# Optimization experiments

Measured on AMD Instinct MI355X. Metric: run time of the kernel, lower is better.

## Reference

```python
import jax, jax.numpy as jnp
import numpy as np

D_MODEL, D_INNER, D_STATE, DT_RANK, D_CONV = 1024, 2048, 16, 64, 4
BATCH, SEQLEN = 2, 2048


def setup_inputs() -> dict:
    key = jax.random.key(0)
    ks = jax.random.split(key, 8)
    g = lambda k, shape, scale: jax.random.normal(k, shape, jnp.float32) * scale
    hidden_states = jax.random.normal(ks[0], (BATCH, SEQLEN, D_MODEL), jnp.float32)
    W_in = g(ks[1], (2 * D_INNER, D_MODEL), D_MODEL ** -0.5)
    conv_w = g(ks[2], (D_INNER, D_CONV), D_CONV ** -0.5)
    conv_b = jnp.zeros((D_INNER,), jnp.float32)
    W_x = g(ks[3], (DT_RANK + 2 * D_STATE, D_INNER), D_INNER ** -0.5)
    dt_init_std = DT_RANK ** -0.5  # dt_scale = 1.0
    W_dt = jax.random.uniform(ks[4], (D_INNER, DT_RANK), jnp.float32, -dt_init_std, dt_init_std)
    # faithful dt bias init: softplus^{-1}(dt) with dt ~ LogUniform(dt_min, dt_max)
    dt = jnp.exp(jax.random.uniform(ks[5], (D_INNER,), jnp.float32)
                 * (np.log(0.1) - np.log(0.001)) + np.log(0.001))
    dt = jnp.clip(dt, 1e-4)
    b_dt = dt + jnp.log(-jnp.expm1(-dt))
    A_log = jnp.log(jnp.broadcast_to(jnp.arange(1, D_STATE + 1, dtype=jnp.float32), (D_INNER, D_STATE)))
    D_param = jnp.ones((D_INNER,), jnp.float32)
    W_out = g(ks[6], (D_MODEL, D_INNER), D_INNER ** -0.5)
    return dict(hidden_states=hidden_states, W_in=W_in, conv_w=conv_w, conv_b=conv_b,
                W_x=W_x, W_dt=W_dt, b_dt=b_dt, A_log=A_log, D_param=D_param, W_out=W_out)


def reference(hidden_states, W_in, conv_w, conv_b, W_x, W_dt, b_dt, A_log, D_param, W_out):
    B_, L, _ = hidden_states.shape
    # in_proj (no bias) then split into x / gate z
    xz = jnp.einsum('bld,ed->ble', hidden_states, W_in)  # (B, L, 2*d_inner)
    x, z = jnp.split(xz, 2, axis=-1)
    # depthwise causal conv1d (padding = d_conv - 1, truncated to L)
    xp = jnp.pad(x, ((0, 0), (D_CONV - 1, 0), (0, 0)))
    xc = conv_b + sum(conv_w[:, k] * xp[:, k:k + L, :] for k in range(D_CONV))
    x = jax.nn.silu(xc)  # (B, L, d_inner)
    # input-dependent SSM params
    A = -jnp.exp(A_log)  # (d_inner, d_state)
    proj = jnp.einsum('bld,ed->ble', x, W_x)
    dt_lo, Bm, Cm = jnp.split(proj, [DT_RANK, DT_RANK + D_STATE], axis=-1)
    dt = jax.nn.softplus(jnp.einsum('blr,dr->bld', dt_lo, W_dt) + b_dt)  # (B, L, d_inner)
    # sequential selective scan: h = exp(dt*A)*h + dt*B*x ; y = C.h + D*x
    def step(h, inp):
        x_t, dt_t, B_t, C_t = inp  # (B,d), (B,d), (B,n), (B,n)
        dA = jnp.exp(dt_t[..., None] * A)                       # (B, d, n)
        h = dA * h + (dt_t * x_t)[..., None] * B_t[:, None, :]  # (B, d, n)
        y_t = jnp.einsum('bdn,bn->bd', h, C_t)
        return h, y_t

    h0 = jnp.zeros((B_, D_INNER, D_STATE), x.dtype)
    xs = (x.swapaxes(0, 1), dt.swapaxes(0, 1), Bm.swapaxes(0, 1), Cm.swapaxes(0, 1))
    _, ys = jax.lax.scan(step, h0, xs)
    y = ys.swapaxes(0, 1) + D_param * x
    y = y * jax.nn.silu(z)
    return jnp.einsum('bld,md->blm', y, W_out)
```

## Files before the change

### kernel.cpp

```cpp
#include <hip/hip_runtime.h>

typedef _Float16 f16;
typedef f16   f16x2 __attribute__((ext_vector_type(2)));
typedef f16   f16x4 __attribute__((ext_vector_type(4)));
typedef f16   f16x8 __attribute__((ext_vector_type(8)));
typedef float f32x2 __attribute__((ext_vector_type(2)));
typedef float f32x4 __attribute__((ext_vector_type(4)));

#define LOG2E 1.44269504088896f

__device__ __forceinline__ float fast_exp(float x) {
    return __builtin_amdgcn_exp2f(x * LOG2E);
}
__device__ __forceinline__ float silu_f(float x) {
    return x / (1.f + __builtin_amdgcn_exp2f(-LOG2E * x));
}
__device__ __forceinline__ float softplus_f(float x) {
    if (x > 16.f) return x;
    float e = __builtin_amdgcn_exp2f(x * LOG2E);
    return __builtin_amdgcn_logf(1.f + e) * 0.69314718056f;
}

#define DPP_ADD(x, ctrl) \
    ((x) + __int_as_float(__builtin_amdgcn_update_dpp(0, __float_as_int(x), (ctrl), 0xF, 0xF, true)))

__device__ __forceinline__ void gload_lds16(const void* g, void* l) {
    __builtin_amdgcn_global_load_lds((__attribute__((address_space(1))) void*)(g),
                                     (__attribute__((address_space(3))) void*)(l), 16, 0, 0);
}

__global__ __launch_bounds__(256) void cvt_all(const float* __restrict__ hidden, const float* __restrict__ W_in,
                                               const float* __restrict__ W_out, const float* __restrict__ W_dt,
                                               const float* __restrict__ W_x,
                                               f16* __restrict__ h16, f16* __restrict__ Win16,
                                               f16* __restrict__ Wout16, f16* __restrict__ Wdt16,
                                               f16* __restrict__ Wx16) {
    int i = blockIdx.x * 256 + threadIdx.x;
    const float* src;
    f16* dst;
    int idx;
    if (i < 1048576) { src = hidden; dst = h16; idx = i; }
    else if (i < 2097152) { src = W_in; dst = Win16; idx = i - 1048576; }
    else if (i < 2621440) { src = W_out; dst = Wout16; idx = i - 2097152; }
    else if (i < 2654208) { src = W_dt; dst = Wdt16; idx = i - 2621440; }
    else {
        int q = i - 2654208;
        int r = q >> 9;
        f32x4 v = {0.f, 0.f, 0.f, 0.f};
        if (r < 96) v = ((const f32x4*)W_x)[q];
        f16x4 o = {(f16)v[0], (f16)v[1], (f16)v[2], (f16)v[3]};
        ((f16x4*)Wx16)[q] = o;
        return;
    }
    f32x4 v = ((const f32x4*)src)[idx];
    f16x4 o = {(f16)v[0], (f16)v[1], (f16)v[2], (f16)v[3]};
    ((f16x4*)dst)[idx] = o;
}

__global__ void reduce_proj(const f16* __restrict__ Pws, float* __restrict__ proj,
                            f16* __restrict__ dtlo) {
    int i = blockIdx.x * 256 + threadIdx.x;
    int m = i >> 5, c0 = (i & 31) * 4;
    f32x4 s = {0.f, 0.f, 0.f, 0.f};
#pragma unroll
    for (int z = 0; z < 8; z++) {
        f16x4 p = *(const f16x4*)(Pws + (size_t)z * 4096 * 128 + (size_t)m * 128 + c0);
        s += (f32x4){(float)p[0], (float)p[1], (float)p[2], (float)p[3]};
    }
    *(f32x4*)(proj + (size_t)m * 128 + c0) = s;
    if (c0 < 64) {
        f16x4 o = {(f16)s[0], (f16)s[1], (f16)s[2], (f16)s[3]};
        *(f16x4*)(dtlo + (size_t)m * 64 + c0) = o;
    }
}

__global__ __launch_bounds__(1024) void gemm256(const f16* __restrict__ A, const f16* __restrict__ B,
                                                f16* __restrict__ C, int N, int K) {
    __shared__ f16 As[4][256 * 32];
    __shared__ f16 Bs[4][256 * 32];
    const int tid = threadIdx.x;
    const int w = tid >> 6, l = tid & 63;
    const int wr = w >> 2, wc = w & 3;
    const int lrow = l & 15, lkb = l >> 4;
    const int gpos = ((lkb ^ ((lrow >> 1) & 3)) * 8);
    const int bid = blockIdx.y * 16 + blockIdx.x;
    const int wg = (bid & 7) * 32 + (bid >> 3);
    const int mt = wg >> 4, nt = wg & 15;
    const int NT = K >> 5;

    f32x4 acc[4][4];
#pragma unroll
    for (int i = 0; i < 4; i++)
#pragma unroll
        for (int j = 0; j < 4; j++) acc[i][j] = (f32x4){0.f, 0.f, 0.f, 0.f};

    const int srow = w * 16 + (l >> 2);
    const int sgran = (l & 3) ^ ((l >> 3) & 3);
    const f16* Ag = A + (size_t)(mt * 256 + srow) * K + sgran * 8;
    const f16* Bg = B + (size_t)(nt * 256 + srow) * K + sgran * 8;

#define SCALL(s, kt, q)                                        \
    do {                                                       \
        if ((q) == 0) gload_lds16(Ag + (kt), &As[s][w * 512]); \
        if ((q) == 1) gload_lds16(Bg + (kt), &Bs[s][w * 512]); \
    } while (0)

    SCALL(0, 0, 0); SCALL(0, 0, 1);
    SCALL(1, 32, 0); SCALL(1, 32, 1);
    SCALL(2, 64, 0); SCALL(2, 64, 1);

    for (int t = 0; t < NT; ++t) {
        const f16* as = As[t & 3];
        const f16* bs = Bs[t & 3];
        const int pslot = (t + 3) & 3;
        const int pkt = ((t + 3 < NT) ? (t + 3) : (NT - 1)) * 32;

        asm volatile("s_waitcnt vmcnt(4)" ::: "memory");
        __builtin_amdgcn_sched_barrier(0);
        __builtin_amdgcn_s_barrier();
        __builtin_amdgcn_sched_barrier(0);

        f16x8 af[4], bf[4];
#pragma unroll
        for (int i = 0; i < 4; i++)
            af[i] = *(const f16x8*)&as[(wr * 64 + i * 16 + lrow) * 32 + gpos];
#pragma unroll
        for (int j = 0; j < 4; j++)
            bf[j] = *(const f16x8*)&bs[(wc * 64 + j * 16 + lrow) * 32 + gpos];
        SCALL(pslot, pkt, 0);
        SCALL(pslot, pkt, 1);
        __builtin_amdgcn_s_barrier();
        __builtin_amdgcn_sched_barrier(0);
        __builtin_amdgcn_s_setprio(1);
#pragma unroll
        for (int i = 0; i < 4; i++)
#pragma unroll
            for (int j = 0; j < 4; j++)
                acc[i][j] = __builtin_amdgcn_mfma_f32_16x16x32_f16(af[i], bf[j], acc[i][j], 0, 0, 0);
        __builtin_amdgcn_s_setprio(0);
    }
#undef SCALL

    const int orow = mt * 256 + wr * 64 + (l >> 4) * 4;
    const int ocol = nt * 256 + wc * 64 + lrow;
#pragma unroll
    for (int i = 0; i < 4; i++)
#pragma unroll
        for (int j = 0; j < 4; j++)
#pragma unroll
            for (int q = 0; q < 4; q++)
                C[(size_t)(orow + i * 16 + q) * N + ocol + j * 16] = (f16)acc[i][j][q];
}

__global__ __launch_bounds__(512) void gemm_o32(const f16* __restrict__ A, const f16* __restrict__ B,
                                                float* __restrict__ C, int N, int K) {
    __shared__ f16 As[4][128 * 32];
    __shared__ f16 Bs[4][128 * 32];
    const int tid = threadIdx.x;
    const int w = tid >> 6, l = tid & 63;
    const int wr = w >> 2, wc = w & 3;
    const int lrow = l & 15, lkb = l >> 4;
    const int gpos = ((lkb ^ ((lrow >> 1) & 3)) * 8);
    const int bid = blockIdx.y * 8 + blockIdx.x;
    const int wg = (bid & 7) * 32 + (bid >> 3);
    const int nt = wg & 7, mt = wg >> 3;
    const int NT = K >> 5;

    f32x4 acc[4][2];
#pragma unroll
    for (int i = 0; i < 4; i++)
#pragma unroll
        for (int j = 0; j < 2; j++) acc[i][j] = (f32x4){0.f, 0.f, 0.f, 0.f};

    const int srow = w * 16 + (l >> 2);
    const int sgran = (l & 3) ^ ((l >> 3) & 3);
    const f16* Ag = A + (size_t)(mt * 128 + srow) * K + sgran * 8;
    const f16* Bg = B + (size_t)(nt * 128 + srow) * K + sgran * 8;

#define QCALL(s, kt, q)                                        \
    do {                                                       \
        if ((q) == 0) gload_lds16(Ag + (kt), &As[s][w * 512]); \
        if ((q) == 1) gload_lds16(Bg + (kt), &Bs[s][w * 512]); \
    } while (0)

    QCALL(0, 0, 0); QCALL(0, 0, 1);
    QCALL(1, 32, 0); QCALL(1, 32, 1);
    QCALL(2, 64, 0); QCALL(2, 64, 1);

    for (int t = 0; t < NT; ++t) {
        const f16* as = As[t & 3];
        const f16* bs = Bs[t & 3];
        const int pslot = (t + 3) & 3;
        const int pkt = ((t + 3 < NT) ? (t + 3) : (NT - 1)) * 32;

        asm volatile("s_waitcnt vmcnt(4)" ::: "memory");
        __builtin_amdgcn_sched_barrier(0);
        __builtin_amdgcn_s_barrier();
        __builtin_amdgcn_sched_barrier(0);

        f16x8 af[4], bf[2];
#pragma unroll
        for (int i = 0; i < 4; i++)
            af[i] = *(const f16x8*)&as[(wr * 64 + i * 16 + lrow) * 32 + gpos];
#pragma unroll
        for (int j = 0; j < 2; j++)
            bf[j] = *(const f16x8*)&bs[(wc * 32 + j * 16 + lrow) * 32 + gpos];
        QCALL(pslot, pkt, 0);
        QCALL(pslot, pkt, 1);
        __builtin_amdgcn_s_barrier();
        __builtin_amdgcn_sched_barrier(0);
        __builtin_amdgcn_s_setprio(1);
#pragma unroll
        for (int i = 0; i < 4; i++)
#pragma unroll
            for (int j = 0; j < 2; j++)
                acc[i][j] = __builtin_amdgcn_mfma_f32_16x16x32_f16(af[i], bf[j], acc[i][j], 0, 0, 0);
        __builtin_amdgcn_s_setprio(0);
    }
#undef QCALL

    const int orow = mt * 128 + wr * 64 + (l >> 4) * 4;
    const int ocol = nt * 128 + wc * 32 + lrow;
#pragma unroll
    for (int i = 0; i < 4; i++)
#pragma unroll
        for (int j = 0; j < 2; j++)
#pragma unroll
            for (int q = 0; q < 4; q++)
                C[(size_t)(orow + i * 16 + q) * N + ocol + j * 16] = acc[i][j][q];
}

template <int EPI, typename OutT>
__global__ __launch_bounds__(256) void gemm_gl(const f16* __restrict__ A, const f16* __restrict__ B,
                                               OutT* __restrict__ C, const float* __restrict__ bias,
                                               int M, int N, int K, int kstep) {
    __shared__ f16 As[2][128 * 64];
    __shared__ f16 Bs[2][128 * 64];
    const int tid = threadIdx.x;
    const int w = tid >> 6, l = tid & 63;
    const int wm = (w >> 1) * 64, wn = (w & 1) * 64;
    const int lrow = l & 15, lkb = l >> 4;
    const int swzr = lrow & 7;
    const int gx = gridDim.x;
    const int nwg = gx * gridDim.y;
    const int bid = blockIdx.y * gx + blockIdx.x;
    const int wg = (bid & 7) * (nwg >> 3) + (bid >> 3);
    const int nt = wg % gx, mt = wg / gx;
    const int kbeg = blockIdx.z * kstep;
    const int NT = kstep >> 6;
    OutT* Cz = C + (size_t)blockIdx.z * M * N;

    f32x4 acc[4][4];
#pragma unroll
    for (int i = 0; i < 4; i++)
#pragma unroll
        for (int j = 0; j < 4; j++) acc[i][j] = (f32x4){0.f, 0.f, 0.f, 0.f};

    const int srow = w * 32 + (l >> 3);
    const int sgran = (l & 7) ^ (l >> 3);
    const f16* Ag = A + (size_t)(mt * 128 + srow) * K + sgran * 8 + kbeg;
    const f16* Bg = B + (size_t)(nt * 128 + srow) * K + sgran * 8 + kbeg;

#define STAGE128(s, kt)                                                         \
    do {                                                                        \
        _Pragma("unroll")                                                       \
        for (int i = 0; i < 4; ++i) {                                           \
            gload_lds16(Ag + (size_t)(i * 8) * K + (kt), &As[s][(w * 32 + i * 8) * 64]); \
            gload_lds16(Bg + (size_t)(i * 8) * K + (kt), &Bs[s][(w * 32 + i * 8) * 64]); \
        }                                                                       \
    } while (0)

    STAGE128(0, 0);
    __syncthreads();

    int cur = 0;
    for (int t = 0; t < NT; ++t) {
        if (t + 1 < NT) STAGE128(cur ^ 1, (t + 1) * 64);
#pragma unroll
        for (int kk = 0; kk < 64; kk += 32) {
            f16x8 af[4], bf[4];
            const int g = (kk >> 3) + lkb;
#pragma unroll
            for (int i = 0; i < 4; i++) {
                af[i] = *(const f16x8*)&As[cur][(wm + i * 16 + lrow) * 64 + ((g ^ swzr) * 8)];
                bf[i] = *(const f16x8*)&Bs[cur][(wn + i * 16 + lrow) * 64 + ((g ^ swzr) * 8)];
            }
#pragma unroll
            for (int i = 0; i < 4; i++)
#pragma unroll
                for (int j = 0; j < 4; j++)
                    acc[i][j] = __builtin_amdgcn_mfma_f32_16x16x32_f16(af[i], bf[j], acc[i][j], 0, 0, 0);
        }
        __syncthreads();
        cur ^= 1;
    }
#undef STAGE128

    const int orow = mt * 128 + wm + (l >> 4) * 4;
    const int ocol = nt * 128 + wn + lrow;
#pragma unroll
    for (int fm = 0; fm < 4; fm++)
#pragma unroll
        for (int fn = 0; fn < 4; fn++) {
            int c = ocol + fn * 16;
            float bv = (EPI == 1) ? bias[c] : 0.f;
#pragma unroll
            for (int i = 0; i < 4; i++) {
                float v = acc[fm][fn][i];
                if (EPI == 1) v = softplus_f(v + bv);
                Cz[(size_t)(orow + fm * 16 + i) * N + c] = (OutT)v;
            }
        }
}

__global__ __launch_bounds__(256) void conv_silu_k(const f16* __restrict__ xz, const float* __restrict__ cw,
                                                   const float* __restrict__ cb, f16* __restrict__ xc) {
    const int d0 = threadIdx.x * 8;
    const int g = blockIdx.x;
    const int b = g >> 9;
    const int l0 = (g & 511) * 4;
    const size_t mrow = (size_t)b * 2048 + l0;
    f32x4 cwv[8];
    float r0[8];
#pragma unroll
    for (int j = 0; j < 8; j++) {
        r0[j] = cb[d0 + j];
        cwv[j] = *(const f32x4*)(cw + (size_t)(d0 + j) * 4);
    }
    const f16x8 zero = {(f16)0.f, (f16)0.f, (f16)0.f, (f16)0.f, (f16)0.f, (f16)0.f, (f16)0.f, (f16)0.f};
    f16x8 xv[7];
#pragma unroll
    for (int i = 0; i < 7; ++i) {
        int ls = l0 - 3 + i;
        xv[i] = (ls >= 0) ? *(const f16x8*)(xz + (mrow - 3 + i) * 4096 + d0) : zero;
    }
#pragma unroll
    for (int tt = 0; tt < 4; ++tt) {
        float r[8];
#pragma unroll
        for (int j = 0; j < 8; j++) r[j] = r0[j];
#pragma unroll
        for (int k = 0; k < 4; k++)
#pragma unroll
            for (int j = 0; j < 8; j++) r[j] += cwv[j][k] * (float)xv[tt + k][j];
        f16x8 o;
#pragma unroll
        for (int j = 0; j < 8; j++) o[j] = (f16)silu_f(r[j]);
        *(f16x8*)(xc + (mrow + tt) * 2048 + d0) = o;
    }
}

#define CT 32
#define NCHUNK 64
#define NSTATE 65536

__global__ __launch_bounds__(128) void scan_p1(const f16* __restrict__ dt16, const f16* __restrict__ xc,
                                               const float* __restrict__ proj, const float* __restrict__ A_log,
                                               f16* __restrict__ Pbuf, f16* __restrict__ Hend) {
    __shared__ float du_s[CT][32];
    __shared__ float bq_s[CT][20];
    const int tid = threadIdx.x;
    const int c = blockIdx.x, dg = blockIdx.y, b = blockIdx.z;
    const int d_base = dg << 5;
    const int g = tid >> 2, n = tid & 3;
    const int d = d_base + g;
    const float a0 = -fast_exp(A_log[d * 16 + n]) * LOG2E;
    const float a1 = -fast_exp(A_log[d * 16 + n + 4]) * LOG2E;
    const float a2 = -fast_exp(A_log[d * 16 + n + 8]) * LOG2E;
    const float a3 = -fast_exp(A_log[d * 16 + n + 12]) * LOG2E;
    const size_t mb = (size_t)b * 2048 + (size_t)c * CT;

    {
        const int trow = tid >> 2, seg = tid & 3, j0 = seg * 8;
        const size_t row = mb + trow;
        f16x8 dt8 = *(const f16x8*)(dt16 + row * 2048 + d_base + j0);
        f16x8 xc8 = *(const f16x8*)(xc + row * 2048 + d_base + j0);
#pragma unroll
        for (int k = 0; k < 8; ++k) {
            union { f16x2 h2; float f; } u;
            u.h2[0] = dt8[k];
            u.h2[1] = (f16)((float)dt8[k] * (float)xc8[k]);
            du_s[trow][j0 + k] = u.f;
        }
        f32x4 p0 = *(const f32x4*)(proj + row * 128 + 64 + seg * 4);
#pragma unroll
        for (int k = 0; k < 4; ++k) bq_s[trow][k * 4 + seg] = p0[k];
    }
    __syncthreads();

    float h0 = 0.f, h1 = 0.f, h2 = 0.f, h3 = 0.f, sdt = 0.f;
#pragma unroll 8
    for (int t = 0; t < CT; ++t) {
        union { float f; f16x2 h2; } u;
        u.f = du_s[t][g];
        float dtv = (float)u.h2[0], uv = (float)u.h2[1];
        f32x4 B4 = *(const f32x4*)&bq_s[t][n * 4];
        sdt += dtv;
        h0 = fmaf(__builtin_amdgcn_exp2f(dtv * a0), h0, uv * B4[0]);
        h1 = fmaf(__builtin_amdgcn_exp2f(dtv * a1), h1, uv * B4[1]);
        h2 = fmaf(__builtin_amdgcn_exp2f(dtv * a2), h2, uv * B4[2]);
        h3 = fmaf(__builtin_amdgcn_exp2f(dtv * a3), h3, uv * B4[3]);
    }
    const size_t base = (size_t)c * NSTATE + (size_t)(((b << 11) + d) * 16 + n * 4);
    f16x4 Pv = {(f16)__builtin_amdgcn_exp2f(a0 * sdt), (f16)__builtin_amdgcn_exp2f(a1 * sdt),
                (f16)__builtin_amdgcn_exp2f(a2 * sdt), (f16)__builtin_amdgcn_exp2f(a3 * sdt)};
    f16x4 Ev = {(f16)h0, (f16)h1, (f16)h2, (f16)h3};
    *(f16x4*)(Pbuf + base) = Pv;
    *(f16x4*)(Hend + base) = Ev;
}

__global__ __launch_bounds__(256) void scan_combine(const f16* __restrict__ Pbuf, const f16* __restrict__ Hend,
                                                    f16* __restrict__ Hinit) {
    int s = blockIdx.x * 256 + threadIdx.x;
    float h = 0.f;
#pragma unroll
    for (int c = 0; c < NCHUNK; c++) {
        size_t o = (size_t)c * NSTATE + s;
        Hinit[o] = (f16)h;
        h = fmaf((float)Pbuf[o], h, (float)Hend[o]);
    }
}

__global__ __launch_bounds__(128) void scan_p2(const f16* __restrict__ dt16, const f16* __restrict__ xc,
                                               const f16* __restrict__ xz, const float* __restrict__ proj,
                                               const float* __restrict__ A_log, const float* __restrict__ Dp,
                                               const f16* __restrict__ Hinit, f16* __restrict__ y16) {
    __shared__ f32x2 dg_s[CT][32];
    __shared__ float bq_s[CT][20];
    __shared__ float cq_s[CT][20];
    const int tid = threadIdx.x;
    const int c = blockIdx.x, dg = blockIdx.y, b = blockIdx.z;
    const int d_base = dg << 5;
    const int g = tid >> 2, n = tid & 3;
    const int d = d_base + g;
    const float a0 = -fast_exp(A_log[d * 16 + n]) * LOG2E;
    const float a1 = -fast_exp(A_log[d * 16 + n + 4]) * LOG2E;
    const float a2 = -fast_exp(A_log[d * 16 + n + 8]) * LOG2E;
    const float a3 = -fast_exp(A_log[d * 16 + n + 12]) * LOG2E;
    const size_t mb = (size_t)b * 2048 + (size_t)c * CT;

    {
        const int trow = tid >> 2, seg = tid & 3, j0 = seg * 8;
        const size_t row = mb + trow;
        f16x8 dt8 = *(const f16x8*)(dt16 + row * 2048 + d_base + j0);
        f16x8 xc8 = *(const f16x8*)(xc + row * 2048 + d_base + j0);
        f16x8 xz8 = *(const f16x8*)(xz + row * 4096 + 2048 + d_base + j0);
        f32x4 dv0 = *(const f32x4*)(Dp + d_base + j0);
        f32x4 dv1 = *(const f32x4*)(Dp + d_base + j0 + 4);
#pragma unroll
        for (int k = 0; k < 8; ++k) {
            float dtv = (float)dt8[k], xv = (float)xc8[k];
            union { f16x2 h2; float f; } u;
            u.h2[0] = dt8[k];
            u.h2[1] = (f16)(dtv * xv);
            float sz = silu_f((float)xz8[k]);
            float Dv = (k < 4) ? dv0[k & 3] : dv1[k & 3];
            union { f16x2 h2; float f; } v;
            v.h2[0] = (f16)sz;
            v.h2[1] = (f16)(Dv * xv * sz);
            dg_s[trow][j0 + k] = (f32x2){u.f, v.f};
        }
        f32x4 pb0 = *(const f32x4*)(proj + row * 128 + 64 + seg * 4);
        f32x4 pc0 = *(const f32x4*)(proj + row * 128 + 80 + seg * 4);
#pragma unroll
        for (int k = 0; k < 4; ++k) {
            bq_s[trow][k * 4 + seg] = pb0[k];
            cq_s[trow][k * 4 + seg] = pc0[k];
        }
    }
    const size_t base = (size_t)c * NSTATE + (size_t)(((b << 11) + d) * 16 + n * 4);
    f16x4 H4 = *(const f16x4*)(Hinit + base);
    float h0 = (float)H4[0], h1 = (float)H4[1], h2 = (float)H4[2], h3 = (float)H4[3];
    __syncthreads();

#pragma unroll 8
    for (int t = 0; t < CT; ++t) {
        f32x2 dgv = dg_s[t][g];
        union { float f; f16x2 h2; } u;
        u.f = dgv[0];
        float dtv = (float)u.h2[0], uv = (float)u.h2[1];
        f32x4 B4 = *(const f32x4*)&bq_s[t][n * 4];
        f32x4 C4 = *(const f32x4*)&cq_s[t][n * 4];
        h0 = fmaf(__builtin_amdgcn_exp2f(dtv * a0), h0, uv * B4[0]);
        h1 = fmaf(__builtin_amdgcn_exp2f(dtv * a1), h1, uv * B4[1]);
        h2 = fmaf(__builtin_amdgcn_exp2f(dtv * a2), h2, uv * B4[2]);
        h3 = fmaf(__builtin_amdgcn_exp2f(dtv * a3), h3, uv * B4[3]);
        float yp = h0 * C4[0];
        yp = fmaf(h1, C4[1], yp);
        yp = fmaf(h2, C4[2], yp);
        yp = fmaf(h3, C4[3], yp);
        yp = DPP_ADD(yp, 0xB1);
        yp = DPP_ADD(yp, 0x4E);
        union { float f; f16x2 h2; } v;
        v.f = dgv[1];
        float yv = fmaf(yp, (float)v.h2[0], (float)v.h2[1]);
        if (n == 0) y16[(mb + t) * 2048 + d] = (f16)yv;
    }
}

extern "C" void kernel_launch(void* const* d_in, const int* in_sizes, int n_in,
                              void* d_out, int out_size, void* d_ws, size_t ws_size,
                              hipStream_t stream) {
    const float* hidden = (const float*)d_in[0];
    const float* W_in   = (const float*)d_in[1];
    const float* conv_w = (const float*)d_in[2];
    const float* conv_b = (const float*)d_in[3];
    const float* W_x    = (const float*)d_in[4];
    const float* W_dt   = (const float*)d_in[5];
    const float* b_dt   = (const float*)d_in[6];
    const float* A_log  = (const float*)d_in[7];
    const float* D_par  = (const float*)d_in[8];
    const float* W_out  = (const float*)d_in[9];
    float* out = (float*)d_out;

    char* ws = (char*)d_ws;
    size_t off = 0;
    auto alloc = [&](size_t bytes) { void* p = ws + off; off += (bytes + 255) & ~(size_t)255; return p; };
    f16* h16     = (f16*)alloc(4096ull * 1024 * 2);
    f16* Win16   = (f16*)alloc(4096ull * 1024 * 2);
    f16* Wx16    = (f16*)alloc(128ull * 2048 * 2);
    f16* Wdt16   = (f16*)alloc(2048ull * 64 * 2);
    f16* Wout16  = (f16*)alloc(1024ull * 2048 * 2);
    f16* xz16    = (f16*)alloc(4096ull * 4096 * 2);
    f16* xc16    = (f16*)alloc(4096ull * 2048 * 2);
    float* proj  = (float*)alloc(4096ull * 128 * 4);
    f16* dtlo16  = (f16*)alloc(4096ull * 64 * 2);
    f16* dt16    = (f16*)alloc(4096ull * 2048 * 2);
    f16* y16     = (f16*)alloc(4096ull * 2048 * 2);
    f16* Pws     = (f16*)y16;
    f16* Pbuf16  = (f16*)h16;
    f16* Hend16  = (f16*)y16;
    f16* Hinit16 = (f16*)Win16;
    (void)ws_size; (void)in_sizes; (void)n_in; (void)out_size;

    cvt_all<<<10624, 256, 0, stream>>>(hidden, W_in, W_out, W_dt, W_x,
                                       h16, Win16, Wout16, Wdt16, Wx16);

    gemm256<<<dim3(16, 16), 1024, 0, stream>>>(h16, Win16, xz16, 4096, 1024);
    conv_silu_k<<<1024, 256, 0, stream>>>(xz16, conv_w, conv_b, xc16);
    gemm_gl<0, f16><<<dim3(1, 32, 8), 256, 0, stream>>>(xc16, Wx16, Pws, nullptr, 4096, 128, 2048, 256);
    reduce_proj<<<512, 256, 0, stream>>>(Pws, proj, dtlo16);
    gemm_gl<1, f16><<<dim3(16, 32, 1), 256, 0, stream>>>(dtlo16, Wdt16, dt16, b_dt, 4096, 2048, 64, 64);
    scan_p1<<<dim3(NCHUNK, 64, 2), 128, 0, stream>>>(dt16, xc16, proj, A_log, Pbuf16, Hend16);
    scan_combine<<<256, 256, 0, stream>>>(Pbuf16, Hend16, Hinit16);
    scan_p2<<<dim3(NCHUNK, 64, 2), 128, 0, stream>>>(dt16, xc16, xz16, proj, A_log, D_par, Hinit16, y16);
    gemm_o32<<<dim3(8, 32), 512, 0, stream>>>(y16, Wout16, out, 1024, 2048);
}
```

Measured before the change: 176.5 us.

## Remap scan kernels to one thread per channel holding all 16 states

The chunked scan passes now give each thread one inner channel and all 16 state values in registers, instead of four threads per channel holding four states each. This removes the cross-lane DPP reduction for y, lets every lane write its output, and uses wider vector stores for chunk states, with B/C read as broadcast LDS loads. In exchange there are 4x fewer threads (64-thread blocks, 4096 blocks of one wave each), more registers per thread and less latency hiding.

```diff
diff --git a/kernel.cpp b/kernel.cpp
--- a/kernel.cpp
+++ b/kernel.cpp
@@ -20,9 +20,6 @@
     float e = __builtin_amdgcn_exp2f(x * LOG2E);
     return __builtin_amdgcn_logf(1.f + e) * 0.69314718056f;
 }
-
-#define DPP_ADD(x, ctrl) \
-    ((x) + __int_as_float(__builtin_amdgcn_update_dpp(0, __float_as_int(x), (ctrl), 0xF, 0xF, true)))
 
 __device__ __forceinline__ void gload_lds16(const void* g, void* l) {
     __builtin_amdgcn_global_load_lds((__attribute__((address_space(1))) void*)(g),
@@ -354,59 +351,80 @@
 #define NCHUNK 64
 #define NSTATE 65536
 
-__global__ __launch_bounds__(128) void scan_p1(const f16* __restrict__ dt16, const f16* __restrict__ xc,
-                                               const float* __restrict__ proj, const float* __restrict__ A_log,
-                                               f16* __restrict__ Pbuf, f16* __restrict__ Hend) {
-    __shared__ float du_s[CT][32];
-    __shared__ float bq_s[CT][20];
-    const int tid = threadIdx.x;
-    const int c = blockIdx.x, dg = blockIdx.y, b = blockIdx.z;
-    const int d_base = dg << 5;
-    const int g = tid >> 2, n = tid & 3;
-    const int d = d_base + g;
-    const float a0 = -fast_exp(A_log[d * 16 + n]) * LOG2E;
-    const float a1 = -fast_exp(A_log[d * 16 + n + 4]) * LOG2E;
-    const float a2 = -fast_exp(A_log[d * 16 + n + 8]) * LOG2E;
-    const float a3 = -fast_exp(A_log[d * 16 + n + 12]) * LOG2E;
+__global__ __launch_bounds__(64) void scan_p1(const f16* __restrict__ dt16, const f16* __restrict__ xc,
+                                              const float* __restrict__ proj, const float* __restrict__ A_log,
+                                              f16* __restrict__ Pbuf, f16* __restrict__ Hend) {
+    __shared__ float du_s[CT][64];
+    __shared__ float bq_s[CT][16];
+    const int l = threadIdx.x;
+    const int c = blockIdx.x, dgb = blockIdx.y, b = blockIdx.z;
+    const int d_base = dgb << 6;
+    const int d = d_base + l;
     const size_t mb = (size_t)b * 2048 + (size_t)c * CT;
 
-    {
-        const int trow = tid >> 2, seg = tid & 3, j0 = seg * 8;
-        const size_t row = mb + trow;
-        f16x8 dt8 = *(const f16x8*)(dt16 + row * 2048 + d_base + j0);
-        f16x8 xc8 = *(const f16x8*)(xc + row * 2048 + d_base + j0);
+    float a[16];
+#pragma unroll
+    for (int i = 0; i < 16; i += 4) {
+        f32x4 av = *(const f32x4*)(A_log + (size_t)d * 16 + i);
+#pragma unroll
+        for (int k = 0; k < 4; ++k) a[i + k] = -fast_exp(av[k]) * LOG2E;
+    }
+#pragma unroll
+    for (int i = 0; i < 4; ++i) {
+        int idx = i * 64 + l, row = idx >> 3, j0 = (idx & 7) * 8;
+        size_t r = mb + row;
+        f16x8 dt8 = *(const f16x8*)(dt16 + r * 2048 + d_base + j0);
+        f16x8 xc8 = *(const f16x8*)(xc + r * 2048 + d_base + j0);
 #pragma unroll
         for (int k = 0; k < 8; ++k) {
             union { f16x2 h2; float f; } u;
             u.h2[0] = dt8[k];
             u.h2[1] = (f16)((float)dt8[k] * (float)xc8[k]);
-            du_s[trow][j0 + k] = u.f;
+            du_s[row][j0 + k] = u.f;
         }
-        f32x4 p0 = *(const f32x4*)(proj + row * 128 + 64 + seg * 4);
-#pragma unroll
-        for (int k = 0; k < 4; ++k) bq_s[trow][k * 4 + seg] = p0[k];
+    }
+#pragma unroll
+    for (int i = 0; i < 2; ++i) {
+        int idx = i * 64 + l, row = idx >> 2, s4 = (idx & 3) * 4;
+        *(f32x4*)&bq_s[row][s4] = *(const f32x4*)(proj + (mb + row) * 128 + 64 + s4);
     }
     __syncthreads();
 
-    float h0 = 0.f, h1 = 0.f, h2 = 0.f, h3 = 0.f, sdt = 0.f;
-#pragma unroll 8
+    float h[16];
+#pragma unroll
+    for (int i = 0; i < 16; ++i) h[i] = 0.f;
+    float sdt = 0.f;
+#pragma unroll 2
     for (int t = 0; t < CT; ++t) {
         union { float f; f16x2 h2; } u;
-        u.f = du_s[t][g];
+        u.f = du_s[t][l];
         float dtv = (float)u.h2[0], uv = (float)u.h2[1];
-        f32x4 B4 = *(const f32x4*)&bq_s[t][n * 4];
         sdt += dtv;
-        h0 = fmaf(__builtin_amdgcn_exp2f(dtv * a0), h0, uv * B4[0]);
-        h1 = fmaf(__builtin_amdgcn_exp2f(dtv * a1), h1, uv * B4[1]);
-        h2 = fmaf(__builtin_amdgcn_exp2f(dtv * a2), h2, uv * B4[2]);
-        h3 = fmaf(__builtin_amdgcn_exp2f(dtv * a3), h3, uv * B4[3]);
-    }
-    const size_t base = (size_t)c * NSTATE + (size_t)(((b << 11) + d) * 16 + n * 4);
-    f16x4 Pv = {(f16)__builtin_amdgcn_exp2f(a0 * sdt), (f16)__builtin_amdgcn_exp2f(a1 * sdt),
-                (f16)__builtin_amdgcn_exp2f(a2 * sdt), (f16)__builtin_amdgcn_exp2f(a3 * sdt)};
-    f16x4 Ev = {(f16)h0, (f16)h1, (f16)h2, (f16)h3};
-    *(f16x4*)(Pbuf + base) = Pv;
-    *(f16x4*)(Hend + base) = Ev;
+        f32x4 B0 = *(const f32x4*)&bq_s[t][0];
+        f32x4 B1 = *(const f32x4*)&bq_s[t][4];
+        f32x4 B2 = *(const f32x4*)&bq_s[t][8];
+        f32x4 B3 = *(const f32x4*)&bq_s[t][12];
+#pragma unroll
+        for (int i = 0; i < 4; ++i) {
+            h[i]      = fmaf(__builtin_amdgcn_exp2f(dtv * a[i]),      h[i],      uv * B0[i]);
+            h[i + 4]  = fmaf(__builtin_amdgcn_exp2f(dtv * a[i + 4]),  h[i + 4],  uv * B1[i]);
+            h[i + 8]  = fmaf(__builtin_amdgcn_exp2f(dtv * a[i + 8]),  h[i + 8],  uv * B2[i]);
+            h[i + 12] = fmaf(__builtin_amdgcn_exp2f(dtv * a[i + 12]), h[i + 12], uv * B3[i]);
+        }
+    }
+    const size_t base = (size_t)c * NSTATE + ((size_t)((b << 11) + d) << 4);
+    f16x8 P0, P1, E0, E1;
+#pragma unroll
+    for (int i = 0; i < 8; ++i) {
+        P0[i] = (f16)__builtin_amdgcn_exp2f(a[i] * sdt);
+        P1[i] = (f16)__builtin_amdgcn_exp2f(a[i + 8] * sdt);
+        E0[i] = (f16)h[i];
+        E1[i] = (f16)h[i + 8];
+    }
+    *(f16x8*)(Pbuf + base) = P0;
+    *(f16x8*)(Pbuf + base + 8) = P1;
+    *(f16x8*)(Hend + base) = E0;
+    *(f16x8*)(Hend + base + 8) = E1;
 }
 
 __global__ __launch_bounds__(256) void scan_combine(const f16* __restrict__ Pbuf, const f16* __restrict__ Hend,
@@ -421,30 +439,33 @@
     }
 }
 
-__global__ __launch_bounds__(128) void scan_p2(const f16* __restrict__ dt16, const f16* __restrict__ xc,
-                                               const f16* __restrict__ xz, const float* __restrict__ proj,
-                                               const float* __restrict__ A_log, const float* __restrict__ Dp,
-                                               const f16* __restrict__ Hinit, f16* __restrict__ y16) {
-    __shared__ f32x2 dg_s[CT][32];
-    __shared__ float bq_s[CT][20];
-    __shared__ float cq_s[CT][20];
-    const int tid = threadIdx.x;
-    const int c = blockIdx.x, dg = blockIdx.y, b = blockIdx.z;
-    const int d_base = dg << 5;
-    const int g = tid >> 2, n = tid & 3;
-    const int d = d_base + g;
-    const float a0 = -fast_exp(A_log[d * 16 + n]) * LOG2E;
-    const float a1 = -fast_exp(A_log[d * 16 + n + 4]) * LOG2E;
-    const float a2 = -fast_exp(A_log[d * 16 + n + 8]) * LOG2E;
-    const float a3 = -fast_exp(A_log[d * 16 + n + 12]) * LOG2E;
+__global__ __launch_bounds__(64) void scan_p2(const f16* __restrict__ dt16, const f16* __restrict__ xc,
+                                              const f16* __restrict__ xz, const float* __restrict__ proj,
+                                              const float* __restrict__ A_log, const float* __restrict__ Dp,
+                                              const f16* __restrict__ Hinit, f16* __restrict__ y16) {
+    __shared__ f32x2 dg_s[CT][64];
+    __shared__ float bq_s[CT][16];
+    __shared__ float cq_s[CT][16];
+    const int l = threadIdx.x;
+    const int c = blockIdx.x, dgb = blockIdx.y, b = blockIdx.z;
+    const int d_base = dgb << 6;
+    const int d = d_base + l;
     const size_t mb = (size_t)b * 2048 + (size_t)c * CT;
 
-    {
-        const int trow = tid >> 2, seg = tid & 3, j0 = seg * 8;
-        const size_t row = mb + trow;
-        f16x8 dt8 = *(const f16x8*)(dt16 + row * 2048 + d_base + j0);
-        f16x8 xc8 = *(const f16x8*)(xc + row * 2048 + d_base + j0);
-        f16x8 xz8 = *(const f16x8*)(xz + row * 4096 + 2048 + d_base + j0);
+    float a[16];
+#pragma unroll
+    for (int i = 0; i < 16; i += 4) {
+        f32x4 av = *(const f32x4*)(A_log + (size_t)d * 16 + i);
+#pragma unroll
+        for (int k = 0; k < 4; ++k) a[i + k] = -fast_exp(av[k]) * LOG2E;
+    }
+#pragma unroll
+    for (int i = 0; i < 4; ++i) {
+        int idx = i * 64 + l, row = idx >> 3, j0 = (idx & 7) * 8;
+        size_t r = mb + row;
+        f16x8 dt8 = *(const f16x8*)(dt16 + r * 2048 + d_base + j0);
+        f16x8 xc8 = *(const f16x8*)(xc + r * 2048 + d_base + j0);
+        f16x8 xz8 = *(const f16x8*)(xz + r * 4096 + 2048 + d_base + j0);
         f32x4 dv0 = *(const f32x4*)(Dp + d_base + j0);
         f32x4 dv1 = *(const f32x4*)(Dp + d_base + j0 + 4);
 #pragma unroll
@@ -458,43 +479,54 @@
             union { f16x2 h2; float f; } v;
             v.h2[0] = (f16)sz;
             v.h2[1] = (f16)(Dv * xv * sz);
-            dg_s[trow][j0 + k] = (f32x2){u.f, v.f};
+            dg_s[row][j0 + k] = (f32x2){u.f, v.f};
         }
-        f32x4 pb0 = *(const f32x4*)(proj + row * 128 + 64 + seg * 4);
-        f32x4 pc0 = *(const f32x4*)(proj + row * 128 + 80 + seg * 4);
-#pragma unroll
-        for (int k = 0; k < 4; ++k) {
-            bq_s[trow][k * 4 + seg] = pb0[k];
-            cq_s[trow][k * 4 + seg] = pc0[k];
-        }
-    }
-    const size_t base = (size_t)c * NSTATE + (size_t)(((b << 11) + d) * 16 + n * 4);
-    f16x4 H4 = *(const f16x4*)(Hinit + base);
-    float h0 = (float)H4[0], h1 = (float)H4[1], h2 = (float)H4[2], h3 = (float)H4[3];
+    }
+#pragma unroll
+    for (int i = 0; i < 2; ++i) {
+        int idx = i * 64 + l, row = idx >> 2, s4 = (idx & 3) * 4;
+        *(f32x4*)&bq_s[row][s4] = *(const f32x4*)(proj + (mb + row) * 128 + 64 + s4);
+        *(f32x4*)&cq_s[row][s4] = *(const f32x4*)(proj + (mb + row) * 128 + 80 + s4);
+    }
+    const size_t base = (size_t)c * NSTATE + ((size_t)((b << 11) + d) << 4);
+    f16x8 H0 = *(const f16x8*)(Hinit + base);
+    f16x8 H1 = *(const f16x8*)(Hinit + base + 8);
+    float h[16];
+#pragma unroll
+    for (int i = 0; i < 8; ++i) { h[i] = (float)H0[i]; h[i + 8] = (float)H1[i]; }
     __syncthreads();
 
-#pragma unroll 8
+#pragma unroll 2
     for (int t = 0; t < CT; ++t) {
-        f32x2 dgv = dg_s[t][g];
+        f32x2 dgv = dg_s[t][l];
         union { float f; f16x2 h2; } u;
         u.f = dgv[0];
         float dtv = (float)u.h2[0], uv = (float)u.h2[1];
-        f32x4 B4 = *(const f32x4*)&bq_s[t][n * 4];
-        f32x4 C4 = *(const f32x4*)&cq_s[t][n * 4];
-        h0 = fmaf(__builtin_amdgcn_exp2f(dtv * a0), h0, uv * B4[0]);
-        h1 = fmaf(__builtin_amdgcn_exp2f(dtv * a1), h1, uv * B4[1]);
-        h2 = fmaf(__builtin_amdgcn_exp2f(dtv * a2), h2, uv * B4[2]);
-        h3 = fmaf(__builtin_amdgcn_exp2f(dtv * a3), h3, uv * B4[3]);
-        float yp = h0 * C4[0];
-        yp = fmaf(h1, C4[1], yp);
-        yp = fmaf(h2, C4[2], yp);
-        yp = fmaf(h3, C4[3], yp);
-        yp = DPP_ADD(yp, 0xB1);
-        yp = DPP_ADD(yp, 0x4E);
+        f32x4 B0 = *(const f32x4*)&bq_s[t][0];
+        f32x4 B1 = *(const f32x4*)&bq_s[t][4];
+        f32x4 B2 = *(const f32x4*)&bq_s[t][8];
+        f32x4 B3 = *(const f32x4*)&bq_s[t][12];
+        f32x4 C0 = *(const f32x4*)&cq_s[t][0];
+        f32x4 C1 = *(const f32x4*)&cq_s[t][4];
+        f32x4 C2 = *(const f32x4*)&cq_s[t][8];
+        f32x4 C3 = *(const f32x4*)&cq_s[t][12];
+        float yp0 = 0.f, yp1 = 0.f, yp2 = 0.f, yp3 = 0.f;
+#pragma unroll
+        for (int i = 0; i < 4; ++i) {
+            h[i]      = fmaf(__builtin_amdgcn_exp2f(dtv * a[i]),      h[i],      uv * B0[i]);
+            h[i + 4]  = fmaf(__builtin_amdgcn_exp2f(dtv * a[i + 4]),  h[i + 4],  uv * B1[i]);
+            h[i + 8]  = fmaf(__builtin_amdgcn_exp2f(dtv * a[i + 8]),  h[i + 8],  uv * B2[i]);
+            h[i + 12] = fmaf(__builtin_amdgcn_exp2f(dtv * a[i + 12]), h[i + 12], uv * B3[i]);
+            yp0 = fmaf(h[i], C0[i], yp0);
+            yp1 = fmaf(h[i + 4], C1[i], yp1);
+            yp2 = fmaf(h[i + 8], C2[i], yp2);
+            yp3 = fmaf(h[i + 12], C3[i], yp3);
+        }
+        float yp = (yp0 + yp1) + (yp2 + yp3);
         union { float f; f16x2 h2; } v;
         v.f = dgv[1];
         float yv = fmaf(yp, (float)v.h2[0], (float)v.h2[1]);
-        if (n == 0) y16[(mb + t) * 2048 + d] = (f16)yv;
+        y16[(mb + t) * 2048 + d] = (f16)yv;
     }
 }
 
@@ -541,8 +573,8 @@
     gemm_gl<0, f16><<<dim3(1, 32, 8), 256, 0, stream>>>(xc16, Wx16, Pws, nullptr, 4096, 128, 2048, 256);
     reduce_proj<<<512, 256, 0, stream>>>(Pws, proj, dtlo16);
     gemm_gl<1, f16><<<dim3(16, 32, 1), 256, 0, stream>>>(dtlo16, Wdt16, dt16, b_dt, 4096, 2048, 64, 64);
-    scan_p1<<<dim3(NCHUNK, 64, 2), 128, 0, stream>>>(dt16, xc16, proj, A_log, Pbuf16, Hend16);
+    scan_p1<<<dim3(NCHUNK, 32, 2), 64, 0, stream>>>(dt16, xc16, proj, A_log, Pbuf16, Hend16);
     scan_combine<<<256, 256, 0, stream>>>(Pbuf16, Hend16, Hinit16);
-    scan_p2<<<dim3(NCHUNK, 64, 2), 128, 0, stream>>>(dt16, xc16, xz16, proj, A_log, D_par, Hinit16, y16);
+    scan_p2<<<dim3(NCHUNK, 32, 2), 64, 0, stream>>>(dt16, xc16, xz16, proj, A_log, D_par, Hinit16, y16);
     gemm_o32<<<dim3(8, 32), 512, 0, stream>>>(y16, Wout16, out, 1024, 2048);
 }
```

After: 175.7 us (median of 2 runs). About the same (-0.5%).
